# Performance work log

Hardware: AMD Instinct MI355X
Metric: run time of the kernel (lower is better)

The kernel has to match this reference:

```python
import jax, jax.numpy as jnp
import numpy as np

N_ATOMS = 200000
AEV_DIM = 384
H1, H2, H3 = 160, 128, 96
N_SPECIES = 4
ALPHA = 0.1  # CELU alpha used by ANI atomic networks


def setup_inputs() -> dict:
    key = jax.random.key(0)
    ks = jax.random.split(key, 8)
    aev = jax.random.normal(ks[0], (N_ATOMS, AEV_DIM), dtype=jnp.float32)
    # Disjoint species partition (matches (species==s).nonzero() buffers)
    perm = jax.random.permutation(ks[1], N_ATOMS)
    chunk = N_ATOMS // N_SPECIES
    H_idx = perm[0 * chunk:1 * chunk]
    C_idx = perm[1 * chunk:2 * chunk]
    N_idx = perm[2 * chunk:3 * chunk]
    O_idx = perm[3 * chunk:4 * chunk]

    def init(k, shape, fan_in):
        return (jax.random.normal(k, shape, dtype=jnp.float32) / np.float32(np.sqrt(fan_in)))

    # Stacked per-species MLP params: leading axis = species (H,C,N,O)
    W1 = init(ks[2], (N_SPECIES, AEV_DIM, H1), AEV_DIM); b1 = jnp.zeros((N_SPECIES, H1), jnp.float32)
    W2 = init(ks[3], (N_SPECIES, H1, H2), H1);          b2 = jnp.zeros((N_SPECIES, H2), jnp.float32)
    W3 = init(ks[4], (N_SPECIES, H2, H3), H2);          b3 = jnp.zeros((N_SPECIES, H3), jnp.float32)
    W4 = init(ks[5], (N_SPECIES, H3, 1), H3);           b4 = jnp.zeros((N_SPECIES, 1), jnp.float32)
    return {"aev": aev,
            "W1": W1, "b1": b1, "W2": W2, "b2": b2,
            "W3": W3, "b3": b3, "W4": W4, "b4": b4,
            "H_idx": H_idx, "C_idx": C_idx, "N_idx": N_idx, "O_idx": O_idx}


def _species_mlp(x, W1, b1, W2, b2, W3, b3, W4, b4):
    h = jax.nn.celu(x @ W1 + b1, ALPHA)
    h = jax.nn.celu(h @ W2 + b2, ALPHA)
    h = jax.nn.celu(h @ W3 + b3, ALPHA)
    return (h @ W4 + b4).reshape(-1)  # per-atom scalar energy


def reference(aev, W1, b1, W2, b2, W3, b3, W4, b4, H_idx, C_idx, N_idx, O_idx):
    out = jnp.zeros((aev.shape[0],), dtype=aev.dtype)
    # Fixed small loop over the 4 species networks (structurally distinct experts)
    for s, idx in enumerate((H_idx, C_idx, N_idx, O_idx)):
        e = _species_mlp(aev[idx], W1[s], b1[s], W2[s], b2[s], W3[s], b3[s], W4[s], b4[s])
        out = out.at[idx].add(e)  # index_add_ scatter
    # output.unsqueeze(0).sum(dim=1) -> molecular energy, shape [1]
    return out[None, :].sum(axis=1)
```

## Files before the change

### kernel.cpp

```cpp
#include <hip/hip_runtime.h>

#define DI __device__ __forceinline__

constexpr int AEV = 384;
constexpr int H1N = 160;
constexpr int H2N = 128;
constexpr int H3N = 96;
constexpr int NSP = 4;
constexpr int TM  = 128;
constexpr int SP1 = 168;
constexpr int SP2 = 136;
constexpr int SP3 = 104;
constexpr int KP  = 104;

using short8  = __attribute__((ext_vector_type(8))) short;
using short4v = __attribute__((ext_vector_type(4))) short;
using f32x4   = __attribute__((ext_vector_type(4))) float;

__device__ short g_w1h[NSP * H1N * AEV];
__device__ short g_w1l[NSP * H1N * AEV];
__device__ short g_w2h[NSP * H2N * H1N];
__device__ short g_w2l[NSP * H2N * H1N];
__device__ short g_w3h[NSP * H3N * H2N];
__device__ short g_w3l[NSP * H3N * H2N];

DI short f2bf(float f) {
  unsigned u = __float_as_uint(f);
  u += 0x7fffu + ((u >> 16) & 1u);
  return (short)(u >> 16);
}
DI float bf2f(short h) {
  return __uint_as_float(((unsigned)(unsigned short)h) << 16);
}
DI float celu_f(float x) {
  return fmaxf(x, 0.f) + 0.1f * (exp2f(fminf(x, 0.f) * 14.426950408889634f) - 1.f);
}
DI f32x4 mfma16(short8 a, short8 b, f32x4 c) {
  return __builtin_amdgcn_mfma_f32_16x16x32_bf16(a, b, c, 0, 0, 0);
}

__global__ void wt_build(const float* __restrict__ src, int which, int K, int N) {
  short* dh = (which == 0) ? g_w1h : (which == 1) ? g_w2h : g_w3h;
  short* dl = (which == 0) ? g_w1l : (which == 1) ? g_w2l : g_w3l;
  int id = blockIdx.x * 256 + threadIdx.x;
  int per = K * N;
  if (id >= NSP * per) return;
  int s = id / per, r = id - s * per;
  int n = r / K, k = r - n * K;
  float v = src[s * per + k * N + n];
  short h = f2bf(v);
  dh[s * per + n * K + k] = h;
  dl[s * per + n * K + k] = f2bf(v - bf2f(h));
}

template <int MT, int K>
DI void layer_lds(const short* __restrict__ wtH, const short* __restrict__ wtL,
                  const short* Hsrc, int SPs, short* Hdst, int SPd,
                  const float* biasL, short* WTb,
                  int tid, int l15, int quad, int wav) {
  constexpr int N = MT * 16;
  f32x4 acc[MT][2];
#pragma unroll
  for (int m = 0; m < MT; ++m)
#pragma unroll
    for (int nt = 0; nt < 2; ++nt)
#pragma unroll
      for (int i = 0; i < 4; ++i) acc[m][nt][i] = 0.f;

#pragma unroll
  for (int c = 0; c < 2; ++c) {
    const int Kc  = (c == 0) ? 96 : (K - 96);
    const int kc0 = (c == 0) ? 0 : 96;
    const int CH  = Kc / 8;
    const int ITERS = (2 * N * CH) / 256;
    short8 wreg[12];
#pragma unroll
    for (int ii = 0; ii < ITERS; ++ii) {
      int i = ii * 256 + tid;
      int c16 = i % CH; int t2 = i / CH; int n = t2 % N; int pol = t2 / N;
      wreg[ii] = *(const short8*)((pol ? wtL : wtH) + n * K + kc0 + c16 * 8);
    }
    __syncthreads();
#pragma unroll
    for (int ii = 0; ii < ITERS; ++ii) {
      int i = ii * 256 + tid;
      int c16 = i % CH; int t2 = i / CH; int n = t2 % N; int pol = t2 / N;
      *(short8*)(WTb + pol * (N * KP) + n * KP + c16 * 8) = wreg[ii];
    }
    __syncthreads();
    const int nks = Kc / 32;
    for (int ks = 0; ks < nks; ++ks) {
      const int kl = ks * 32 + quad * 8;
      short8 b[2];
#pragma unroll
      for (int nt = 0; nt < 2; ++nt)
        b[nt] = *(const short8*)(Hsrc + (wav * 32 + nt * 16 + l15) * SPs + kc0 + kl);
#pragma unroll
      for (int mt = 0; mt < MT; ++mt) {
        short8 ah = *(const short8*)(WTb + (mt * 16 + l15) * KP + kl);
        short8 al = *(const short8*)(WTb + N * KP + (mt * 16 + l15) * KP + kl);
#pragma unroll
        for (int nt = 0; nt < 2; ++nt) {
          acc[mt][nt] = mfma16(ah, b[nt], acc[mt][nt]);
          acc[mt][nt] = mfma16(al, b[nt], acc[mt][nt]);
        }
      }
    }
  }
#pragma unroll
  for (int mt = 0; mt < MT; ++mt)
#pragma unroll
    for (int nt = 0; nt < 2; ++nt) {
      int nb = mt * 16 + quad * 4;
      int atom = wav * 32 + nt * 16 + l15;
      short4v o;
#pragma unroll
      for (int j = 0; j < 4; ++j) o[j] = f2bf(celu_f(acc[mt][nt][j] + biasL[nb + j]));
      *(short4v*)(Hdst + atom * SPd + nb) = o;
    }
}

__global__ __launch_bounds__(256, 1) void fused_mlp(
    const float* __restrict__ aev,
    const float* __restrict__ b1, const float* __restrict__ b2,
    const float* __restrict__ b3,
    const float* __restrict__ W4, const float* __restrict__ pb4,
    const int* __restrict__ i0, const int* __restrict__ i1,
    const int* __restrict__ i2, const int* __restrict__ i3,
    int chunk, float* __restrict__ out) {
  __shared__ short WTb[2 * H1N * KP];
  __shared__ short H1s[TM * SP1];
  __shared__ short H2s[TM * SP2];
  __shared__ float BIAS1[H1N];
  __shared__ float BIAS2[H2N];
  __shared__ float BIAS3[H3N];
  __shared__ float RED[4];

  const int tid  = threadIdx.x;
  const int lane = tid & 63, wav = tid >> 6;
  const int l15  = lane & 15, quad = lane >> 4;
  const int s    = blockIdx.y;
  const int tile = blockIdx.x;
  const int* idx = (s == 0) ? i0 : (s == 1) ? i1 : (s == 2) ? i2 : i3;

  if (tid < H1N) BIAS1[tid] = b1[s * H1N + tid];
  if (tid < H2N) BIAS2[tid] = b2[s * H2N + tid];
  if (tid < H3N) BIAS3[tid] = b3[s * H3N + tid];

  const short* w1h = g_w1h + s * H1N * AEV; const short* w1l = g_w1l + s * H1N * AEV;
  const short* w2h = g_w2h + s * H2N * H1N; const short* w2l = g_w2l + s * H2N * H1N;
  const short* w3h = g_w3h + s * H3N * H2N; const short* w3l = g_w3l + s * H3N * H2N;

  const int a0 = tile * TM + wav * 32 + l15;
  const int a1 = a0 + 16;
  const int r0 = idx[a0 < chunk ? a0 : (chunk - 1)];
  const int r1 = idx[a1 < chunk ? a1 : (chunk - 1)];
  const float* xrow0 = aev + (size_t)r0 * AEV + quad * 8;
  const float* xrow1 = aev + (size_t)r1 * AEV + quad * 8;

  f32x4 acc[10][2];
#pragma unroll
  for (int m = 0; m < 10; ++m)
#pragma unroll
    for (int nt = 0; nt < 2; ++nt)
#pragma unroll
      for (int i = 0; i < 4; ++i) acc[m][nt][i] = 0.f;

#pragma unroll
  for (int c = 0; c < 4; ++c) {
    const int kc0 = c * 96;
    float4 xg[3][2][2];
#pragma unroll
    for (int ks = 0; ks < 3; ++ks)
#pragma unroll
      for (int nt = 0; nt < 2; ++nt) {
        const float* p = (nt ? xrow1 : xrow0) + kc0 + ks * 32;
        xg[ks][nt][0] = *(const float4*)p;
        xg[ks][nt][1] = *(const float4*)(p + 4);
      }
    short8 wreg[15];
#pragma unroll
    for (int ii = 0; ii < 15; ++ii) {
      int i = ii * 256 + tid;
      int c16 = i % 12; int t2 = i / 12; int n = t2 % H1N; int pol = t2 / H1N;
      wreg[ii] = *(const short8*)((pol ? w1l : w1h) + n * AEV + kc0 + c16 * 8);
    }
    __syncthreads();
#pragma unroll
    for (int ii = 0; ii < 15; ++ii) {
      int i = ii * 256 + tid;
      int c16 = i % 12; int t2 = i / 12; int n = t2 % H1N; int pol = t2 / H1N;
      *(short8*)(WTb + pol * (H1N * KP) + n * KP + c16 * 8) = wreg[ii];
    }
    __syncthreads();
#pragma unroll
    for (int ks = 0; ks < 3; ++ks) {
      short8 b[2];
#pragma unroll
      for (int nt = 0; nt < 2; ++nt) {
        float4 A = xg[ks][nt][0], B = xg[ks][nt][1];
        short8 t;
        t[0] = f2bf(A.x); t[1] = f2bf(A.y); t[2] = f2bf(A.z); t[3] = f2bf(A.w);
        t[4] = f2bf(B.x); t[5] = f2bf(B.y); t[6] = f2bf(B.z); t[7] = f2bf(B.w);
        b[nt] = t;
      }
      const int kl = ks * 32 + quad * 8;
#pragma unroll
      for (int mt = 0; mt < 10; ++mt) {
        short8 ah = *(const short8*)(WTb + (mt * 16 + l15) * KP + kl);
        short8 al = *(const short8*)(WTb + H1N * KP + (mt * 16 + l15) * KP + kl);
#pragma unroll
        for (int nt = 0; nt < 2; ++nt) {
          acc[mt][nt] = mfma16(ah, b[nt], acc[mt][nt]);
          acc[mt][nt] = mfma16(al, b[nt], acc[mt][nt]);
        }
      }
    }
  }
#pragma unroll
  for (int mt = 0; mt < 10; ++mt)
#pragma unroll
    for (int nt = 0; nt < 2; ++nt) {
      int nb = mt * 16 + quad * 4;
      int atom = wav * 32 + nt * 16 + l15;
      short4v o;
#pragma unroll
      for (int j = 0; j < 4; ++j) o[j] = f2bf(celu_f(acc[mt][nt][j] + BIAS1[nb + j]));
      *(short4v*)(H1s + atom * SP1 + nb) = o;
    }

  layer_lds<8, 160>(w2h, w2l, H1s, SP1, H2s, SP2, BIAS2, WTb, tid, l15, quad, wav);
  layer_lds<6, 128>(w3h, w3l, H2s, SP2, H1s, SP3, BIAS3, WTb, tid, l15, quad, wav);
  __syncthreads();

  float e = 0.f;
  if (tid < TM) {
    const short* h3 = H1s + tid * SP3;
    const float* w4 = W4 + s * H3N;
    float sum = 0.f;
#pragma unroll
    for (int j = 0; j < H3N; ++j) sum += bf2f(h3[j]) * w4[j];
    if (tile * TM + tid < chunk) e = sum + pb4[s];
  }
#pragma unroll
  for (int off = 32; off > 0; off >>= 1) e += __shfl_down(e, off, 64);
  if (lane == 0) RED[wav] = e;
  __syncthreads();
  if (tid == 0) atomicAdd(out, RED[0] + RED[1] + RED[2] + RED[3]);
}

extern "C" void kernel_launch(void* const* d_in, const int* in_sizes, int n_in,
                              void* d_out, int out_size, void* d_ws, size_t ws_size,
                              hipStream_t stream) {
  (void)n_in; (void)d_ws; (void)ws_size;
  const float* aev = (const float*)d_in[0];
  const float* W1  = (const float*)d_in[1];
  const float* b1  = (const float*)d_in[2];
  const float* W2  = (const float*)d_in[3];
  const float* b2  = (const float*)d_in[4];
  const float* W3  = (const float*)d_in[5];
  const float* b3  = (const float*)d_in[6];
  const float* W4  = (const float*)d_in[7];
  const float* b4  = (const float*)d_in[8];
  const int* iH = (const int*)d_in[9];
  const int* iC = (const int*)d_in[10];
  const int* iN = (const int*)d_in[11];
  const int* iO = (const int*)d_in[12];
  const int chunk = in_sizes[9];

  hipMemsetAsync(d_out, 0, out_size * sizeof(float), stream);
  wt_build<<<(NSP * AEV * H1N + 255) / 256, 256, 0, stream>>>(W1, 0, AEV, H1N);
  wt_build<<<(NSP * H1N * H2N + 255) / 256, 256, 0, stream>>>(W2, 1, H1N, H2N);
  wt_build<<<(NSP * H2N * H3N + 255) / 256, 256, 0, stream>>>(W3, 2, H2N, H3N);

  const int tiles = (chunk + TM - 1) / TM;
  dim3 grid(tiles, NSP);
  fused_mlp<<<grid, 256, 0, stream>>>(aev, b1, b2, b3, W4, b4,
                                      iH, iC, iN, iO, chunk, (float*)d_out);
}
```

Baseline: 563.4 us.

## Read MLP weight fragments directly from global memory, drop LDS weight staging

Removes the LDS staging of weight tiles, which needed two barriers per chunk. Each wave now loads its bf16 hi/lo weight fragments straight from global memory, where they are expected to be cache-resident, and bias is read from global too. The freed LDS together with launch_bounds(256,2) allows two blocks per CU. It also prefetches the next AEV chunk into registers, fuses the three weight-transpose kernels and the output memset into one prep launch, and vectorizes the final dot product. The cost is that every wave re-reads the weights from L2/L1 instead of sharing one LDS copy, and register pressure rises.

```diff
diff --git a/kernel.cpp b/kernel.cpp
--- a/kernel.cpp
+++ b/kernel.cpp
@@ -11,18 +11,17 @@
 constexpr int SP1 = 168;
 constexpr int SP2 = 136;
 constexpr int SP3 = 104;
-constexpr int KP  = 104;
 
 using short8  = __attribute__((ext_vector_type(8))) short;
 using short4v = __attribute__((ext_vector_type(4))) short;
 using f32x4   = __attribute__((ext_vector_type(4))) float;
 
-__device__ short g_w1h[NSP * H1N * AEV];
-__device__ short g_w1l[NSP * H1N * AEV];
-__device__ short g_w2h[NSP * H2N * H1N];
-__device__ short g_w2l[NSP * H2N * H1N];
-__device__ short g_w3h[NSP * H3N * H2N];
-__device__ short g_w3l[NSP * H3N * H2N];
+__device__ __align__(16) short g_w1h[NSP * H1N * AEV];
+__device__ __align__(16) short g_w1l[NSP * H1N * AEV];
+__device__ __align__(16) short g_w2h[NSP * H2N * H1N];
+__device__ __align__(16) short g_w2l[NSP * H2N * H1N];
+__device__ __align__(16) short g_w3h[NSP * H3N * H2N];
+__device__ __align__(16) short g_w3l[NSP * H3N * H2N];
 
 DI short f2bf(float f) {
   unsigned u = __float_as_uint(f);
@@ -39,26 +38,35 @@
   return __builtin_amdgcn_mfma_f32_16x16x32_bf16(a, b, c, 0, 0, 0);
 }
 
-__global__ void wt_build(const float* __restrict__ src, int which, int K, int N) {
-  short* dh = (which == 0) ? g_w1h : (which == 1) ? g_w2h : g_w3h;
-  short* dl = (which == 0) ? g_w1l : (which == 1) ? g_w2l : g_w3l;
-  int id = blockIdx.x * 256 + threadIdx.x;
-  int per = K * N;
-  if (id >= NSP * per) return;
-  int s = id / per, r = id - s * per;
-  int n = r / K, k = r - n * K;
+template <int K, int N>
+DI void tp(const float* __restrict__ src, short* dh, short* dl, int id) {
+  constexpr int per = K * N;
+  int s = id / per, r = id % per;
+  int n = r / K, k = r % K;
   float v = src[s * per + k * N + n];
   short h = f2bf(v);
   dh[s * per + n * K + k] = h;
   dl[s * per + n * K + k] = f2bf(v - bf2f(h));
 }
 
+__global__ void prep(const float* __restrict__ W1, const float* __restrict__ W2,
+                     const float* __restrict__ W3, float* __restrict__ out) {
+  int id = blockIdx.x * 256 + threadIdx.x;
+  if (id == 0) out[0] = 0.f;
+  constexpr int E1 = NSP * AEV * H1N;
+  constexpr int E2 = NSP * H1N * H2N;
+  constexpr int E3 = NSP * H2N * H3N;
+  if (id < E1)            tp<AEV, H1N>(W1, g_w1h, g_w1l, id);
+  else if (id < E1 + E2)  tp<H1N, H2N>(W2, g_w2h, g_w2l, id - E1);
+  else if (id < E1 + E2 + E3) tp<H2N, H3N>(W3, g_w3h, g_w3l, id - E1 - E2);
+}
+
 template <int MT, int K>
 DI void layer_lds(const short* __restrict__ wtH, const short* __restrict__ wtL,
                   const short* Hsrc, int SPs, short* Hdst, int SPd,
-                  const float* biasL, short* WTb,
-                  int tid, int l15, int quad, int wav) {
-  constexpr int N = MT * 16;
+                  const float* __restrict__ biasG,
+                  int l15, int quad, int wav) {
+  constexpr int NKS = K / 32;
   f32x4 acc[MT][2];
 #pragma unroll
   for (int m = 0; m < MT; ++m)
@@ -67,60 +75,45 @@
 #pragma unroll
       for (int i = 0; i < 4; ++i) acc[m][nt][i] = 0.f;
 
-#pragma unroll
-  for (int c = 0; c < 2; ++c) {
-    const int Kc  = (c == 0) ? 96 : (K - 96);
-    const int kc0 = (c == 0) ? 0 : 96;
-    const int CH  = Kc / 8;
-    const int ITERS = (2 * N * CH) / 256;
-    short8 wreg[12];
-#pragma unroll
-    for (int ii = 0; ii < ITERS; ++ii) {
-      int i = ii * 256 + tid;
-      int c16 = i % CH; int t2 = i / CH; int n = t2 % N; int pol = t2 / N;
-      wreg[ii] = *(const short8*)((pol ? wtL : wtH) + n * K + kc0 + c16 * 8);
-    }
-    __syncthreads();
-#pragma unroll
-    for (int ii = 0; ii < ITERS; ++ii) {
-      int i = ii * 256 + tid;
-      int c16 = i % CH; int t2 = i / CH; int n = t2 % N; int pol = t2 / N;
-      *(short8*)(WTb + pol * (N * KP) + n * KP + c16 * 8) = wreg[ii];
-    }
-    __syncthreads();
-    const int nks = Kc / 32;
-    for (int ks = 0; ks < nks; ++ks) {
-      const int kl = ks * 32 + quad * 8;
-      short8 b[2];
-#pragma unroll
-      for (int nt = 0; nt < 2; ++nt)
-        b[nt] = *(const short8*)(Hsrc + (wav * 32 + nt * 16 + l15) * SPs + kc0 + kl);
-#pragma unroll
-      for (int mt = 0; mt < MT; ++mt) {
-        short8 ah = *(const short8*)(WTb + (mt * 16 + l15) * KP + kl);
-        short8 al = *(const short8*)(WTb + N * KP + (mt * 16 + l15) * KP + kl);
-#pragma unroll
-        for (int nt = 0; nt < 2; ++nt) {
-          acc[mt][nt] = mfma16(ah, b[nt], acc[mt][nt]);
-          acc[mt][nt] = mfma16(al, b[nt], acc[mt][nt]);
-        }
-      }
-    }
-  }
-#pragma unroll
-  for (int mt = 0; mt < MT; ++mt)
+  short8 b[NKS][2];
+#pragma unroll
+  for (int ks = 0; ks < NKS; ++ks)
+#pragma unroll
+    for (int nt = 0; nt < 2; ++nt)
+      b[ks][nt] = *(const short8*)(Hsrc + (wav * 32 + nt * 16 + l15) * SPs + ks * 32 + quad * 8);
+
+#pragma unroll
+  for (int mt = 0; mt < MT; ++mt) {
+    const short* ph = wtH + (mt * 16 + l15) * K + quad * 8;
+    const short* pl = wtL + (mt * 16 + l15) * K + quad * 8;
+#pragma unroll
+    for (int ks = 0; ks < NKS; ++ks) {
+      short8 ah = *(const short8*)(ph + ks * 32);
+      short8 al = *(const short8*)(pl + ks * 32);
+#pragma unroll
+      for (int nt = 0; nt < 2; ++nt) {
+        acc[mt][nt] = mfma16(ah, b[ks][nt], acc[mt][nt]);
+        acc[mt][nt] = mfma16(al, b[ks][nt], acc[mt][nt]);
+      }
+    }
+  }
+#pragma unroll
+  for (int mt = 0; mt < MT; ++mt) {
+    float4 bb = *(const float4*)(biasG + mt * 16 + quad * 4);
 #pragma unroll
     for (int nt = 0; nt < 2; ++nt) {
-      int nb = mt * 16 + quad * 4;
       int atom = wav * 32 + nt * 16 + l15;
       short4v o;
-#pragma unroll
-      for (int j = 0; j < 4; ++j) o[j] = f2bf(celu_f(acc[mt][nt][j] + biasL[nb + j]));
-      *(short4v*)(Hdst + atom * SPd + nb) = o;
-    }
-}
-
-__global__ __launch_bounds__(256, 1) void fused_mlp(
+      o[0] = f2bf(celu_f(acc[mt][nt][0] + bb.x));
+      o[1] = f2bf(celu_f(acc[mt][nt][1] + bb.y));
+      o[2] = f2bf(celu_f(acc[mt][nt][2] + bb.z));
+      o[3] = f2bf(celu_f(acc[mt][nt][3] + bb.w));
+      *(short4v*)(Hdst + atom * SPd + mt * 16 + quad * 4) = o;
+    }
+  }
+}
+
+__global__ __launch_bounds__(256, 2) void fused_mlp(
     const float* __restrict__ aev,
     const float* __restrict__ b1, const float* __restrict__ b2,
     const float* __restrict__ b3,
@@ -128,12 +121,8 @@
     const int* __restrict__ i0, const int* __restrict__ i1,
     const int* __restrict__ i2, const int* __restrict__ i3,
     int chunk, float* __restrict__ out) {
-  __shared__ short WTb[2 * H1N * KP];
-  __shared__ short H1s[TM * SP1];
-  __shared__ short H2s[TM * SP2];
-  __shared__ float BIAS1[H1N];
-  __shared__ float BIAS2[H2N];
-  __shared__ float BIAS3[H3N];
+  __shared__ __align__(16) short H1s[TM * SP1];
+  __shared__ __align__(16) short H2s[TM * SP2];
   __shared__ float RED[4];
 
   const int tid  = threadIdx.x;
@@ -143,10 +132,6 @@
   const int tile = blockIdx.x;
   const int* idx = (s == 0) ? i0 : (s == 1) ? i1 : (s == 2) ? i2 : i3;
 
-  if (tid < H1N) BIAS1[tid] = b1[s * H1N + tid];
-  if (tid < H2N) BIAS2[tid] = b2[s * H2N + tid];
-  if (tid < H3N) BIAS3[tid] = b3[s * H3N + tid];
-
   const short* w1h = g_w1h + s * H1N * AEV; const short* w1l = g_w1l + s * H1N * AEV;
   const short* w2h = g_w2h + s * H2N * H1N; const short* w2l = g_w2l + s * H2N * H1N;
   const short* w3h = g_w3h + s * H3N * H2N; const short* w3l = g_w3l + s * H3N * H2N;
@@ -166,71 +151,69 @@
 #pragma unroll
       for (int i = 0; i < 4; ++i) acc[m][nt][i] = 0.f;
 
+  float4 xgf[3][2][2];
+  short8 xb[3][2];
+
+  auto ldx = [&](int c) {
+#pragma unroll
+    for (int ks = 0; ks < 3; ++ks)
+#pragma unroll
+      for (int nt = 0; nt < 2; ++nt) {
+        const float* p = (nt ? xrow1 : xrow0) + c * 96 + ks * 32;
+        xgf[ks][nt][0] = *(const float4*)p;
+        xgf[ks][nt][1] = *(const float4*)(p + 4);
+      }
+  };
+
+  ldx(0);
 #pragma unroll
   for (int c = 0; c < 4; ++c) {
-    const int kc0 = c * 96;
-    float4 xg[3][2][2];
 #pragma unroll
     for (int ks = 0; ks < 3; ++ks)
 #pragma unroll
       for (int nt = 0; nt < 2; ++nt) {
-        const float* p = (nt ? xrow1 : xrow0) + kc0 + ks * 32;
-        xg[ks][nt][0] = *(const float4*)p;
-        xg[ks][nt][1] = *(const float4*)(p + 4);
-      }
-    short8 wreg[15];
-#pragma unroll
-    for (int ii = 0; ii < 15; ++ii) {
-      int i = ii * 256 + tid;
-      int c16 = i % 12; int t2 = i / 12; int n = t2 % H1N; int pol = t2 / H1N;
-      wreg[ii] = *(const short8*)((pol ? w1l : w1h) + n * AEV + kc0 + c16 * 8);
-    }
-    __syncthreads();
-#pragma unroll
-    for (int ii = 0; ii < 15; ++ii) {
-      int i = ii * 256 + tid;
-      int c16 = i % 12; int t2 = i / 12; int n = t2 % H1N; int pol = t2 / H1N;
-      *(short8*)(WTb + pol * (H1N * KP) + n * KP + c16 * 8) = wreg[ii];
-    }
-    __syncthreads();
-#pragma unroll
-    for (int ks = 0; ks < 3; ++ks) {
-      short8 b[2];
-#pragma unroll
-      for (int nt = 0; nt < 2; ++nt) {
-        float4 A = xg[ks][nt][0], B = xg[ks][nt][1];
+        float4 A = xgf[ks][nt][0], B = xgf[ks][nt][1];
         short8 t;
         t[0] = f2bf(A.x); t[1] = f2bf(A.y); t[2] = f2bf(A.z); t[3] = f2bf(A.w);
         t[4] = f2bf(B.x); t[5] = f2bf(B.y); t[6] = f2bf(B.z); t[7] = f2bf(B.w);
-        b[nt] = t;
-      }
-      const int kl = ks * 32 + quad * 8;
-#pragma unroll
-      for (int mt = 0; mt < 10; ++mt) {
-        short8 ah = *(const short8*)(WTb + (mt * 16 + l15) * KP + kl);
-        short8 al = *(const short8*)(WTb + H1N * KP + (mt * 16 + l15) * KP + kl);
+        xb[ks][nt] = t;
+      }
+    if (c < 3) ldx(c + 1);
+#pragma unroll
+    for (int mt = 0; mt < 10; ++mt) {
+      const short* ph = w1h + (mt * 16 + l15) * AEV + c * 96 + quad * 8;
+      const short* pl = w1l + (mt * 16 + l15) * AEV + c * 96 + quad * 8;
+#pragma unroll
+      for (int ks = 0; ks < 3; ++ks) {
+        short8 ah = *(const short8*)(ph + ks * 32);
+        short8 al = *(const short8*)(pl + ks * 32);
 #pragma unroll
         for (int nt = 0; nt < 2; ++nt) {
-          acc[mt][nt] = mfma16(ah, b[nt], acc[mt][nt]);
-          acc[mt][nt] = mfma16(al, b[nt], acc[mt][nt]);
+          acc[mt][nt] = mfma16(ah, xb[ks][nt], acc[mt][nt]);
+          acc[mt][nt] = mfma16(al, xb[ks][nt], acc[mt][nt]);
         }
       }
     }
   }
 #pragma unroll
-  for (int mt = 0; mt < 10; ++mt)
+  for (int mt = 0; mt < 10; ++mt) {
+    float4 bb = *(const float4*)(b1 + s * H1N + mt * 16 + quad * 4);
 #pragma unroll
     for (int nt = 0; nt < 2; ++nt) {
-      int nb = mt * 16 + quad * 4;
       int atom = wav * 32 + nt * 16 + l15;
       short4v o;
-#pragma unroll
-      for (int j = 0; j < 4; ++j) o[j] = f2bf(celu_f(acc[mt][nt][j] + BIAS1[nb + j]));
-      *(short4v*)(H1s + atom * SP1 + nb) = o;
-    }
-
-  layer_lds<8, 160>(w2h, w2l, H1s, SP1, H2s, SP2, BIAS2, WTb, tid, l15, quad, wav);
-  layer_lds<6, 128>(w3h, w3l, H2s, SP2, H1s, SP3, BIAS3, WTb, tid, l15, quad, wav);
+      o[0] = f2bf(celu_f(acc[mt][nt][0] + bb.x));
+      o[1] = f2bf(celu_f(acc[mt][nt][1] + bb.y));
+      o[2] = f2bf(celu_f(acc[mt][nt][2] + bb.z));
+      o[3] = f2bf(celu_f(acc[mt][nt][3] + bb.w));
+      *(short4v*)(H1s + atom * SP1 + mt * 16 + quad * 4) = o;
+    }
+  }
+
+  __syncthreads();
+  layer_lds<8, 160>(w2h, w2l, H1s, SP1, H2s, SP2, b2 + s * H2N, l15, quad, wav);
+  __syncthreads();
+  layer_lds<6, 128>(w3h, w3l, H2s, SP2, H1s, SP3, b3 + s * H3N, l15, quad, wav);
   __syncthreads();
 
   float e = 0.f;
@@ -239,7 +222,13 @@
     const float* w4 = W4 + s * H3N;
     float sum = 0.f;
 #pragma unroll
-    for (int j = 0; j < H3N; ++j) sum += bf2f(h3[j]) * w4[j];
+    for (int j = 0; j < 12; ++j) {
+      short8 h8 = *(const short8*)(h3 + j * 8);
+      float4 wa = *(const float4*)(w4 + j * 8);
+      float4 wb = *(const float4*)(w4 + j * 8 + 4);
+      sum += bf2f(h8[0]) * wa.x + bf2f(h8[1]) * wa.y + bf2f(h8[2]) * wa.z + bf2f(h8[3]) * wa.w
+           + bf2f(h8[4]) * wb.x + bf2f(h8[5]) * wb.y + bf2f(h8[6]) * wb.z + bf2f(h8[7]) * wb.w;
+    }
     if (tile * TM + tid < chunk) e = sum + pb4[s];
   }
 #pragma unroll
@@ -252,7 +241,7 @@
 extern "C" void kernel_launch(void* const* d_in, const int* in_sizes, int n_in,
                               void* d_out, int out_size, void* d_ws, size_t ws_size,
                               hipStream_t stream) {
-  (void)n_in; (void)d_ws; (void)ws_size;
+  (void)n_in; (void)d_ws; (void)ws_size; (void)out_size;
   const float* aev = (const float*)d_in[0];
   const float* W1  = (const float*)d_in[1];
   const float* b1  = (const float*)d_in[2];
@@ -268,10 +257,8 @@
   const int* iO = (const int*)d_in[12];
   const int chunk = in_sizes[9];
 
-  hipMemsetAsync(d_out, 0, out_size * sizeof(float), stream);
-  wt_build<<<(NSP * AEV * H1N + 255) / 256, 256, 0, stream>>>(W1, 0, AEV, H1N);
-  wt_build<<<(NSP * H1N * H2N + 255) / 256, 256, 0, stream>>>(W2, 1, H1N, H2N);
-  wt_build<<<(NSP * H2N * H3N + 255) / 256, 256, 0, stream>>>(W3, 2, H2N, H3N);
+  constexpr int TOT = NSP * (AEV * H1N + H1N * H2N + H2N * H3N);
+  prep<<<TOT / 256, 256, 0, stream>>>(W1, W2, W3, (float*)d_out);
 
   const int tiles = (chunk + TM - 1) / TM;
   dim3 grid(tiles, NSP);
```

Result: slower. 707.7 us (+25.6%).
